# Kernel optimization log

Measured on AMD Instinct MI355X. Metric: run time of the kernel, lower is better.

The kernel has to match this reference:

```python
import jax, jax.numpy as jnp
import numpy as np

N_PARTICLES = 512
N_DIM = 3
N_KERNELS = 32
N_TIME = 10
BATCH = 8
EPS = 1e-6


def rbf_kernels(d, mu, neg_log_gamma, derivative=False):
    # d: [..., 1], mu/neg_log_gamma: [K] -> normalized rbf kernels [..., K]
    inv_gamma2 = jnp.square(jnp.exp(neg_log_gamma))
    diff = d - mu
    rbfs = jnp.exp(-jnp.square(diff) * inv_gamma2)
    srbf = rbfs.sum(-1, keepdims=True)
    kernels = rbfs / (EPS + srbf)
    if not derivative:
        return kernels, None
    drbfs = -2.0 * diff * inv_gamma2 * rbfs
    sdrbf = drbfs.sum(-1, keepdims=True)
    dkernels = drbfs / (EPS + srbf) - rbfs * sdrbf / jnp.square(EPS + srbf)
    return kernels, dkernels


def setup_inputs() -> dict:
    key = jax.random.key(0)
    k_t, k_x, k_w = jax.random.split(key, 3)
    t = jax.random.uniform(k_t, (1,), dtype=jnp.float32)
    x = jax.random.normal(k_x, (BATCH, N_PARTICLES * N_DIM), dtype=jnp.float32)
    mus = jnp.linspace(0.0, 1.0, N_KERNELS, dtype=jnp.float32)
    neg_log_gammas = -jnp.log(jnp.full((N_KERNELS,), 0.3, dtype=jnp.float32))
    mus_time = jnp.linspace(0.0, 1.0, N_TIME, dtype=jnp.float32)
    neg_log_gammas_time = -jnp.log(jnp.full((N_TIME,), 0.3, dtype=jnp.float32))
    weights = jax.random.normal(k_w, (N_KERNELS, N_TIME), dtype=jnp.float32) * np.float32(np.sqrt(1.0 / N_KERNELS))
    bias = jnp.zeros((1, N_TIME), dtype=jnp.float32)
    importance = jnp.zeros((N_KERNELS,), dtype=jnp.float32)
    return dict(t=t, x=x, mus=mus, neg_log_gammas=neg_log_gammas,
                mus_time=mus_time, neg_log_gammas_time=neg_log_gammas_time,
                weights=weights, bias=bias, importance=importance)


def reference(t, x, mus, neg_log_gammas, mus_time, neg_log_gammas_time, weights, bias, importance):
    B = x.shape[0]
    xp = x.reshape(B, N_PARTICLES, N_DIM)
    # pairwise distance vectors r[b,i,j] = x_i - x_j : [B,N,N,D]
    r = xp[:, :, None, :] - xp[:, None, :, :]
    d = jnp.sqrt(jnp.square(r).sum(-1) + EPS)[..., None]          # [B,N,N,1]
    rbfs, d_rbfs = rbf_kernels(d, mus, neg_log_gammas, derivative=True)  # [B,N,N,K]
    force_mag = (rbfs + jnp.square(importance)) @ weights + bias  # [B,N,N,T]
    d_force_mag = d_rbfs @ weights                                # [B,N,N,T]
    trbfs, _ = rbf_kernels(t, mus_time, neg_log_gammas_time)      # [T]
    force_mag = (force_mag * trbfs).sum(-1, keepdims=True)        # [B,N,N,1]
    d_force_mag = (d_force_mag * trbfs).sum(-1, keepdims=True)
    # mask replicates bgflow's remove_diagonal in distance_vectors (self-pairs excluded)
    mask = (1.0 - jnp.eye(N_PARTICLES, dtype=x.dtype))[None, :, :, None]
    forces = (r * force_mag * mask).sum(-2).reshape(B, -1)        # [B, N*D]
    divergence = ((d * d_force_mag + N_DIM * force_mag) * mask).reshape(B, -1).sum(-1, keepdims=True)
    return forces, -divergence
```

## Files before the change

kernel.cpp:

```cpp
#include <hip/hip_runtime.h>

#define N_P   512
#define N_DIMC 3
#define N_K   32
#define N_T   10
#define BATCHC 8
#define EPSC  1e-6f
#define LOG2E 1.4426950408889634f

typedef float f2 __attribute__((ext_vector_type(2)));

__device__ __forceinline__ float rfl(float v) {
    return __int_as_float(__builtin_amdgcn_readfirstlane(__float_as_int(v)));
}


__global__ __launch_bounds__(512, 8) void
pair_kernel(const float* __restrict__ x,
            const float* __restrict__ t,
            const float* __restrict__ mus,
            const float* __restrict__ nlg,
            const float* __restrict__ mus_time,
            const float* __restrict__ nlg_time,
            const float* __restrict__ weights,
            const float* __restrict__ bias,
            const float* __restrict__ importance,
            float* __restrict__ out) {
    const int b     = blockIdx.x >> 7;
    const int itile = blockIdx.x & 127;

    __shared__ float sx[N_P], sy[N_P], sz[N_P];
    __shared__ float cws[41];
    __shared__ float red[8][4];

    const int tid = threadIdx.x;

    const float* xb = x + b * (N_P * N_DIMC);
#pragma unroll
    for (int idx = tid; idx < N_P * N_DIMC; idx += 512) {
        float v = xb[idx];
        int p = idx / 3;
        int c = idx - 3 * p;
        if (c == 0) sx[p] = v;
        else if (c == 1) sy[p] = v;
        else sz[p] = v;
    }

    if (tid < N_K) {
        float im = importance[tid];
        float t0 = t[0];
        float r[N_T];
        float s = 0.f;
        for (int tt = 0; tt < N_T; ++tt) {
            float g = __expf(nlg_time[tt]);
            float diff = t0 - mus_time[tt];
            r[tt] = __expf(-diff * diff * g * g);
            s += r[tt];
        }
        float inv = 1.f / (EPSC + s);
        float w = 0.f;
        for (int tt = 0; tt < N_T; ++tt) w = fmaf(weights[tid * N_T + tt], r[tt] * inv, w);
        int pos = (tid < 16) ? (2 * tid) : (2 * (tid - 16) + 1);
        cws[pos] = w;
        float contrib = im * im * w;
        if (tid == 0) {
            for (int tt = 0; tt < N_T; ++tt) contrib = fmaf(bias[tt], r[tt] * inv, contrib);
        }
#pragma unroll
        for (int off = 16; off >= 1; off >>= 1)
            contrib += __shfl_down(contrib, off, 64);
        if (tid == 0) cws[40] = contrib;
    } else if (tid == 64) {
        float g0 = __expf(nlg[0]);
        float c  = g0 * g0;
        float D  = mus[1] - mus[0];
        float cdd = c * D * D;
        cws[32] = -c * LOG2E;
        cws[33] = 2.f * c * D * LOG2E;
        cws[34] = -2.f * c;
        cws[35] = mus[16];
        cws[36] = D;
        cws[37] = __expf(-cdd);
        cws[38] = __expf(-33.f * cdd);
        cws[39] = __expf(-2.f * cdd);
    }
    __syncthreads();

    f2 w2[16];
#pragma unroll
    for (int k = 0; k < 16; ++k)
        w2[k] = (f2){rfl(cws[2 * k]), rfl(cws[2 * k + 1])};
    const float mcl2  = rfl(cws[32]);
    const float ku    = rfl(cws[33]);
    const float n2c   = rfl(cws[34]);
    const float mu16  = rfl(cws[35]);
    const float dlt   = rfl(cws[36]);
    const float q     = rfl(cws[37]);
    const float q33   = rfl(cws[38]);
    const float qqs   = rfl(cws[39]);
    const float cterm = rfl(cws[40]);
    const f2 qq2 = (f2){qqs, qqs};

    const int wid   = tid >> 6;
    const int lane  = tid & 63;
    const int i     = itile * 4 + (wid & 3);
    const int jbase = (wid >> 2) * (N_P / 2);

    const float xi_x = sx[i], xi_y = sy[i], xi_z = sz[i];

    float fx = 0.f, fy = 0.f, fz = 0.f, dva = 0.f, dvb = 0.f;

    for (int jj = 0; jj < N_P / 2 / 64; ++jj) {
        int j = jbase + jj * 64 + lane;
        float dx = xi_x - sx[j];
        float dy = xi_y - sy[j];
        float dz = xi_z - sz[j];
        float dsq = fmaf(dx, dx, fmaf(dy, dy, dz * dz)) + EPSC;
        float d = __builtin_amdgcn_sqrtf(dsq);

        float dh  = d - mu16;
        float alo = __builtin_amdgcn_exp2f(mcl2 * dsq);
        float ahi = __builtin_amdgcn_exp2f(mcl2 * dh * dh);
        float u   = __builtin_amdgcn_exp2f(ku * d);

        f2 a2    = (f2){alo, ahi};
        f2 m2    = (f2){u * q, u * q33};
        f2 diff2 = (f2){d, dh};
        f2 md2   = (f2){-dlt, -dlt};
        f2 rs = (f2){0.f, 0.f}, wes = rs, dse = rs, wdse = rs;
#pragma unroll
        for (int k = 0; k < 15; ++k) {
            f2 wek = w2[k] * a2;
            rs   += a2;
            wes  += wek;
            dse  += diff2 * a2;
            wdse += diff2 * wek;
            a2    = a2 * m2;
            m2    = m2 * qq2;
            diff2 = diff2 + md2;
        }
        {
            f2 wek = w2[15] * a2;
            rs   += a2;
            wes  += wek;
            dse  += diff2 * a2;
            wdse += diff2 * wek;
        }
        float rsum = rs.x + rs.y;
        float we   = wes.x + wes.y;
        float ds   = dse.x + dse.y;
        float wds  = wdse.x + wdse.y;

        float inv  = __builtin_amdgcn_rcpf(EPSC + rsum);
        float fmag = fmaf(we, inv, cterm);
        float uu   = fmaf(-we * inv, ds, wds);
        float dfm  = (n2c * inv) * uu;

        bool self = (j == i);
        fmag = self ? 0.f : fmag;
        dfm  = self ? 0.f : dfm;

        fx  = fmaf(dx, fmag, fx);
        fy  = fmaf(dy, fmag, fy);
        fz  = fmaf(dz, fmag, fz);
        dva = fmaf(d, dfm, dva);
        dvb += fmag;
    }
    float dv = fmaf(3.f, dvb, dva);

#pragma unroll
    for (int off = 32; off >= 1; off >>= 1) {
        fx += __shfl_down(fx, off, 64);
        fy += __shfl_down(fy, off, 64);
        fz += __shfl_down(fz, off, 64);
        dv += __shfl_down(dv, off, 64);
    }
    if (lane == 0) {
        red[wid][0] = fx; red[wid][1] = fy; red[wid][2] = fz; red[wid][3] = dv;
    }
    __syncthreads();
    if (tid < 4) {
        int tt = tid;
        int ii = itile * 4 + tt;
        float tfx = red[tt][0] + red[tt + 4][0];
        float tfy = red[tt][1] + red[tt + 4][1];
        float tfz = red[tt][2] + red[tt + 4][2];
        float tdv = red[tt][3] + red[tt + 4][3];
        float* outf = out + (b * N_P + ii) * 3;
        outf[0] = tfx;
        outf[1] = tfy;
        outf[2] = tfz;
        atomicAdd(out + BATCHC * N_P * N_DIMC + b, -tdv);
    }
}

extern "C" void kernel_launch(void* const* d_in, const int* in_sizes, int n_in,
                              void* d_out, int out_size, void* d_ws, size_t ws_size,
                              hipStream_t stream) {
    const float* t          = (const float*)d_in[0];
    const float* x          = (const float*)d_in[1];
    const float* mus        = (const float*)d_in[2];
    const float* nlg        = (const float*)d_in[3];
    const float* mus_time   = (const float*)d_in[4];
    const float* nlg_time   = (const float*)d_in[5];
    const float* weights    = (const float*)d_in[6];
    const float* bias       = (const float*)d_in[7];
    const float* importance = (const float*)d_in[8];
    float* out = (float*)d_out;

    pair_kernel<<<BATCHC * (N_P / 4), 512, 0, stream>>>(
        x, t, mus, nlg, mus_time, nlg_time, weights, bias, importance, out);
}
```

Baseline: 87.05 us.

## Exploit pair symmetry to compute each particle pair once with atomic force scatter

Each block now handles two cyclic offsets for all 512 particles, so every unordered pair is evaluated once instead of twice. The reaction force on j goes into shared memory and is combined with the direct force on i. Per-particle results are then atomically added to the global output, and the divergence is doubled to account for the skipped pairs. This halves the exp- and FMA-heavy RBF evaluation. In exchange it adds 128 global atomic adds per output element, relies on the output being pre-zeroed, and adds block-wide syncs inside the loop.

```diff
diff --git a/kernel.cpp b/kernel.cpp
--- a/kernel.cpp
+++ b/kernel.cpp
@@ -26,12 +26,13 @@
             const float* __restrict__ bias,
             const float* __restrict__ importance,
             float* __restrict__ out) {
-    const int b     = blockIdx.x >> 7;
-    const int itile = blockIdx.x & 127;
+    const int b = blockIdx.x >> 7;
+    const int o = blockIdx.x & 127;
 
     __shared__ float sx[N_P], sy[N_P], sz[N_P];
+    __shared__ float jf[3][N_P];
     __shared__ float cws[41];
-    __shared__ float red[8][4];
+    __shared__ float red[8];
 
     const int tid = threadIdx.x;
 
@@ -101,17 +102,19 @@
     const float cterm = rfl(cws[40]);
     const f2 qq2 = (f2){qqs, qqs};
 
-    const int wid   = tid >> 6;
-    const int lane  = tid & 63;
-    const int i     = itile * 4 + (wid & 3);
-    const int jbase = (wid >> 2) * (N_P / 2);
+    const int wid  = tid >> 6;
+    const int lane = tid & 63;
+    const int i    = tid;
+    const int off0 = 2 * o + 1;
 
     const float xi_x = sx[i], xi_y = sy[i], xi_z = sz[i];
 
     float fx = 0.f, fy = 0.f, fz = 0.f, dva = 0.f, dvb = 0.f;
 
-    for (int jj = 0; jj < N_P / 2 / 64; ++jj) {
-        int j = jbase + jj * 64 + lane;
+#pragma unroll
+    for (int s = 0; s < 2; ++s) {
+        const int off = off0 + s;
+        const int j   = (i + off) & (N_P - 1);
         float dx = xi_x - sx[j];
         float dy = xi_y - sy[j];
         float dz = xi_z - sz[j];
@@ -156,40 +159,45 @@
         float uu   = fmaf(-we * inv, ds, wds);
         float dfm  = (n2c * inv) * uu;
 
-        bool self = (j == i);
-        fmag = self ? 0.f : fmag;
-        dfm  = self ? 0.f : dfm;
+        bool valid = (off < 256) || (i < 256);
+        fmag = valid ? fmag : 0.f;
+        dfm  = valid ? dfm : 0.f;
 
         fx  = fmaf(dx, fmag, fx);
         fy  = fmaf(dy, fmag, fy);
         fz  = fmaf(dz, fmag, fz);
         dva = fmaf(d, dfm, dva);
         dvb += fmag;
-    }
-    float dv = fmaf(3.f, dvb, dva);
-
-#pragma unroll
-    for (int off = 32; off >= 1; off >>= 1) {
-        fx += __shfl_down(fx, off, 64);
-        fy += __shfl_down(fy, off, 64);
-        fz += __shfl_down(fz, off, 64);
-        dv += __shfl_down(dv, off, 64);
-    }
-    if (lane == 0) {
-        red[wid][0] = fx; red[wid][1] = fy; red[wid][2] = fz; red[wid][3] = dv;
-    }
+
+        if (s == 0) {
+            jf[0][j] = -dx * fmag;
+            jf[1][j] = -dy * fmag;
+            jf[2][j] = -dz * fmag;
+        } else {
+            jf[0][j] += -dx * fmag;
+            jf[1][j] += -dy * fmag;
+            jf[2][j] += -dz * fmag;
+        }
+        __syncthreads();
+    }
+
+    float dv = 2.f * fmaf(3.f, dvb, dva);
+#pragma unroll
+    for (int offr = 32; offr >= 1; offr >>= 1)
+        dv += __shfl_down(dv, offr, 64);
+    if (lane == 0) red[wid] = dv;
     __syncthreads();
-    if (tid < 4) {
-        int tt = tid;
-        int ii = itile * 4 + tt;
-        float tfx = red[tt][0] + red[tt + 4][0];
-        float tfy = red[tt][1] + red[tt + 4][1];
-        float tfz = red[tt][2] + red[tt + 4][2];
-        float tdv = red[tt][3] + red[tt + 4][3];
-        float* outf = out + (b * N_P + ii) * 3;
-        outf[0] = tfx;
-        outf[1] = tfy;
-        outf[2] = tfz;
+
+    float tfx = fx + jf[0][i];
+    float tfy = fy + jf[1][i];
+    float tfz = fz + jf[2][i];
+    float* outf = out + (b * N_P + i) * 3;
+    unsafeAtomicAdd(outf + 0, tfx);
+    unsafeAtomicAdd(outf + 1, tfy);
+    unsafeAtomicAdd(outf + 2, tfz);
+    if (tid == 0) {
+        float tdv = red[0] + red[1] + red[2] + red[3]
+                  + red[4] + red[5] + red[6] + red[7];
         atomicAdd(out + BATCHC * N_P * N_DIMC + b, -tdv);
     }
 }
@@ -208,6 +216,6 @@
     const float* importance = (const float*)d_in[8];
     float* out = (float*)d_out;
 
-    pair_kernel<<<BATCHC * (N_P / 4), 512, 0, stream>>>(
+    pair_kernel<<<BATCHC * 128, 512, 0, stream>>>(
         x, t, mus, nlg, mus_time, nlg_time, weights, bias, importance, out);
 }
```

New measurement: 100.4 us. 1.15x slower.
